# Optimization experiments

Measured on AMD Instinct MI355X. Metric: run time of the kernel, lower is better.

The kernel has to match this reference:

```python
import jax, jax.numpy as jnp
import numpy as np
from jax import lax

RATIO = 0.25
RADIUS = 0.2
NSAMPLE = 32


def _fps(xyz, S):
    # xyz: [B, N, 3] -> indices [B, S] via farthest point sampling (start at 0)
    B, N, _ = xyz.shape

    def body(carry, _):
        dist, farthest = carry  # dist [B,N], farthest [B]
        centroid = jnp.take_along_axis(xyz, farthest[:, None, None], axis=1)  # [B,1,3]
        d = jnp.sum((xyz - centroid) ** 2, axis=-1)  # [B,N]
        dist = jnp.minimum(dist, d)
        nxt = jnp.argmax(dist, axis=-1).astype(jnp.int32)
        return (dist, nxt), farthest

    init = (jnp.full((B, N), 1e10, dtype=xyz.dtype), jnp.zeros((B,), jnp.int32))
    _, idx = lax.scan(body, init, None, length=S)  # [S, B]
    return idx.T  # [B, S]


def _ball_query(radius, nsample, xyz, new_xyz):
    # xyz: [B,N,3], new_xyz: [B,S,3] -> neighbor indices [B,S,nsample]
    B, N, _ = xyz.shape
    sqr = jnp.sum((new_xyz[:, :, None, :] - xyz[:, None, :, :]) ** 2, axis=-1)  # [B,S,N]
    arange = jnp.arange(N, dtype=jnp.int32)[None, None, :]
    idx = jnp.where(sqr <= radius * radius, arange, N)  # out-of-ball -> sentinel N
    idx = jnp.sort(idx, axis=-1)[:, :, :nsample]  # first nsample in-ball points
    first = idx[:, :, :1]
    idx = jnp.where(idx == N, first, idx)  # pad with first valid neighbor
    return idx


def reference(xyz, features, w1, b1, w2, b2, w3, b3):
    # xyz: [B,N,3]; features unused in the non-group_all branch (faithful to source).
    B, N, _ = xyz.shape
    S = int(RATIO * N)

    fps_idx = _fps(xyz, S)  # [B,S]
    new_xyz = jnp.take_along_axis(xyz, fps_idx[:, :, None], axis=1)  # [B,S,3]

    nbr_idx = _ball_query(RADIUS, NSAMPLE, xyz, new_xyz)  # [B,S,K]
    b_idx = jnp.arange(B, dtype=jnp.int32)[:, None, None]
    grouped = xyz[b_idx, nbr_idx]  # [B,S,K,3]
    rel = grouped - new_xyz[:, :, None, :]  # center-relative coords

    # new_points.permute(0,3,2,1): [B,S,K,C] -> [B,C,K,S]; shared 1x1 conv MLP + ReLU
    x = rel.transpose(0, 3, 2, 1)  # [B,3,K,S]
    x = jax.nn.relu(jnp.einsum('bcks,oc->boks', x, w1) + b1[None, :, None, None])
    x = jax.nn.relu(jnp.einsum('bcks,oc->boks', x, w2) + b2[None, :, None, None])
    x = jax.nn.relu(jnp.einsum('bcks,oc->boks', x, w3) + b3[None, :, None, None])

    new_points = jnp.max(x, axis=2)  # max over nsample -> [B,128,S]
    return new_xyz.transpose(0, 2, 1), new_points  # [B,3,S], [B,128,S]


def setup_inputs() -> dict:
    key = jax.random.key(0)
    ks = jax.random.split(key, 8)
    B, N = 8, 8192
    xyz = jax.random.uniform(ks[0], (B, N, 3), dtype=jnp.float32)
    features = jax.random.normal(ks[1], (B, 64, N), dtype=jnp.float32)
    w1 = jax.random.normal(ks[2], (64, 3), dtype=jnp.float32) * (1.0 / np.sqrt(3))
    b1 = jnp.zeros((64,), jnp.float32)
    w2 = jax.random.normal(ks[3], (64, 64), dtype=jnp.float32) * (1.0 / np.sqrt(64))
    b2 = jnp.zeros((64,), jnp.float32)
    w3 = jax.random.normal(ks[4], (128, 64), dtype=jnp.float32) * (1.0 / np.sqrt(64))
    b3 = jnp.zeros((128,), jnp.float32)
    return {"xyz": xyz, "features": features, "w1": w1, "b1": b1,
            "w2": w2, "b2": b2, "w3": w3, "b3": b3}
```

## Files before the change

### kernel.cpp

```cpp
#include <hip/hip_runtime.h>
#include <cstdint>
#include <cstddef>

#define BB 8
#define NN 8192
#define SS 2048
#define KNB 32

typedef float f32x2 __attribute__((ext_vector_type(2)));

__device__ __forceinline__ float sqdist_exact(float ax, float ay, float az,
                                              float bx, float by, float bz) {
#pragma clang fp contract(off)
    float dx = ax - bx;
    float dy = ay - by;
    float dz = az - bz;
    return (dx * dx + dy * dy) + dz * dz;
}

__device__ __forceinline__ f32x2 sqdist2_exact(f32x2 px, f32x2 py, f32x2 pz,
                                               f32x2 cx2, f32x2 cy2, f32x2 cz2) {
#pragma clang fp contract(off)
    f32x2 dx = px - cx2;
    f32x2 dy = py - cy2;
    f32x2 dz = pz - cz2;
    return (dx * dx + dy * dy) + dz * dz;
}

__device__ __forceinline__ unsigned long long u64max(unsigned long long a,
                                                     unsigned long long b) {
    return (a > b) ? a : b;
}

template <int CTRL>
__device__ __forceinline__ unsigned long long dpp_u64max_step(unsigned long long k) {
    int lo = __builtin_amdgcn_update_dpp(0, (int)(unsigned)(k & 0xffffffffu),
                                         CTRL, 0xf, 0xf, false);
    int hi = __builtin_amdgcn_update_dpp(0, (int)(unsigned)(k >> 32),
                                         CTRL, 0xf, 0xf, false);
    unsigned long long o = ((unsigned long long)(unsigned)hi << 32) | (unsigned)lo;
    return (o > k) ? o : k;
}
#define ROW_SHR1 0x111
#define ROW_SHR2 0x112
#define ROW_SHR4 0x114
#define ROW_SHR8 0x118
#define ROW_BC15 0x142
#define ROW_BC31 0x143

__device__ __forceinline__ void wave_minmax(float x, float& lo, float& hi) {
    float a = x, b = x;
#pragma unroll
    for (int off = 1; off < 64; off <<= 1) {
        a = fminf(a, __shfl_xor(a, off));
        b = fmaxf(b, __shfl_xor(b, off));
    }
    lo = a;
    hi = b;
}

__global__ void prep_kernel(const float* __restrict__ w1, const float* __restrict__ w2,
                            const float* __restrict__ w3, float* __restrict__ w1T,
                            float* __restrict__ w2T, float* __restrict__ w3T) {
    for (int i = threadIdx.x; i < 192; i += 256) {
        int oc = i / 3, c = i % 3;
        w1T[c * 64 + oc] = w1[i];
    }
    for (int i = threadIdx.x; i < 4096; i += 256) {
        int oc = i >> 6, j = i & 63;
        w2T[j * 64 + oc] = w2[i];
    }
    for (int i = threadIdx.x; i < 8192; i += 256) {
        int oc = i >> 6, j = i & 63;
        w3T[j * 128 + oc] = w3[i];
    }
}

__device__ __forceinline__ int part3(int v) {
    return (v & 1) | ((v & 2) << 2) | ((v & 4) << 4);
}

#define P4_LIST(X) X(0) X(1) X(2) X(3)

__global__ __attribute__((amdgpu_flat_work_group_size(1024, 1024),
                          amdgpu_waves_per_eu(4, 4)))
void fps_kernel(const float* __restrict__ xyz_all,
                float4* __restrict__ wsSorted,
                float4* __restrict__ wsCtr,
                float* __restrict__ out0) {
    const int b = blockIdx.x;
    const float* xyz = xyz_all + (size_t)b * NN * 3;
    float4* sorted = wsSorted + (size_t)b * NN;
    float4* ctr = wsCtr + (size_t)b * SS;
    float* o0 = out0 + (size_t)b * 3 * SS;

    __shared__ float xLds[NN];
    __shared__ float yLds[NN];
    __shared__ float zLds[NN];
    __shared__ float4 ctrLds[SS];
    __shared__ int cellCnt[512];
    __shared__ int cellBase[512];
    __shared__ unsigned long long red[2][16];

    const int tid = threadIdx.x;
    const int wid = tid >> 6;
    const int lane = tid & 63;

    if (tid < 512) cellCnt[tid] = 0;
    __syncthreads();
    int cellReg[8];
#pragma unroll
    for (int j = 0; j < 8; ++j) {
        int p = tid + j * 1024;
        float x = xyz[p * 3 + 0], y = xyz[p * 3 + 1], z = xyz[p * 3 + 2];
        xLds[p] = x; yLds[p] = y; zLds[p] = z;
        int qx = min(7, (int)(x * 8.0f));
        int qy = min(7, (int)(y * 8.0f));
        int qz = min(7, (int)(z * 8.0f));
        cellReg[j] = part3(qx) | (part3(qy) << 1) | (part3(qz) << 2);
        atomicAdd(&cellCnt[cellReg[j]], 1);
    }
    __syncthreads();
    int myCnt = (tid < 512) ? cellCnt[tid] : 0;
    for (int off = 1; off < 512; off <<= 1) {
        int v = (tid < 512 && tid >= off) ? cellCnt[tid - off] : 0;
        __syncthreads();
        if (tid < 512) cellCnt[tid] += v;
        __syncthreads();
    }
    if (tid < 512) cellBase[tid] = cellCnt[tid] - myCnt;
    __syncthreads();
#pragma unroll
    for (int j = 0; j < 8; ++j) {
        int p = tid + j * 1024;
        float x = xLds[p], y = yLds[p], z = zLds[p];
        int pos = atomicAdd(&cellBase[cellReg[j]], 1);
        sorted[pos] = make_float4(x, y, z, __int_as_float(p));
    }
    __threadfence();
    __syncthreads();

#define DECL_PR(j)                                                   \
    f32x2 px##j, py##j, pz##j, dist##j;                              \
    int ndA##j, ndB##j;                                              \
    {                                                                \
        float4 va = sorted[(wid * 8 + 2 * j) * 64 + lane];           \
        float4 vb = sorted[(wid * 8 + 2 * j + 1) * 64 + lane];       \
        px##j = (f32x2){va.x, vb.x};                                 \
        py##j = (f32x2){va.y, vb.y};                                 \
        pz##j = (f32x2){va.z, vb.z};                                 \
        ndA##j = ~__float_as_int(va.w);                              \
        ndB##j = ~__float_as_int(vb.w);                              \
        dist##j = (f32x2){1e10f, 1e10f};                             \
    }
    P4_LIST(DECL_PR)

    float bbxlo = 0.f, bbxhi = 0.f, bbylo = 0.f, bbyhi = 0.f,
          bbzlo = 0.f, bbzhi = 0.f;
#define BRICK_BB2(j)                                              \
    {                                                             \
        float xl, xh, yl, yh, zl, zh;                             \
        wave_minmax(px##j.x, xl, xh);                             \
        wave_minmax(py##j.x, yl, yh);                             \
        wave_minmax(pz##j.x, zl, zh);                             \
        if (lane == 2 * j) {                                      \
            bbxlo = xl; bbxhi = xh;                               \
            bbylo = yl; bbyhi = yh;                               \
            bbzlo = zl; bbzhi = zh;                               \
        }                                                         \
        wave_minmax(px##j.y, xl, xh);                             \
        wave_minmax(py##j.y, yl, yh);                             \
        wave_minmax(pz##j.y, zl, zh);                             \
        if (lane == 2 * j + 1) {                                  \
            bbxlo = xl; bbxhi = xh;                               \
            bbylo = yl; bbyhi = yh;                               \
            bbzlo = zl; bbzhi = zh;                               \
        }                                                         \
    }
    P4_LIST(BRICK_BB2)

    float cx = xLds[0], cy = yLds[0], cz = zLds[0];
    if (tid == 0) ctrLds[0] = make_float4(cx, cy, cz, 0.0f);

    unsigned long long waveKey =
        ((unsigned long long)__float_as_uint(1e10f) << 32) | 0xFFFFFFFFull;
    float wave_bv = 1e10f;

    for (int s = 1; s < SS; ++s) {
        const int par = s & 1;
        float ddx = fmaxf(fmaxf(bbxlo - cx, cx - bbxhi), 0.0f);
        float ddy = fmaxf(fmaxf(bbylo - cy, cy - bbyhi), 0.0f);
        float ddz = fmaxf(fmaxf(bbzlo - cz, cz - bbzhi), 0.0f);
        float lb2 = (ddx * ddx + ddy * ddy) + ddz * ddz;
        bool act = (lane < 8) && (lb2 * 0.999f < wave_bv);
        if (__ballot(act)) {
            const f32x2 c2x = (f32x2){cx, cx};
            const f32x2 c2y = (f32x2){cy, cy};
            const f32x2 c2z = (f32x2){cz, cz};
#define UPD_PR(j)                                                        \
    {                                                                    \
        f32x2 d = sqdist2_exact(px##j, py##j, pz##j, c2x, c2y, c2z);     \
        dist##j.x = fminf(dist##j.x, d.x);                               \
        dist##j.y = fminf(dist##j.y, d.y);                               \
    }
            P4_LIST(UPD_PR)
#define KEY_PR(j)                                                        \
    unsigned long long kA##j =                                           \
        ((unsigned long long)__float_as_uint(dist##j.x) << 32) |         \
        (unsigned)ndA##j;                                                \
    unsigned long long kB##j =                                           \
        ((unsigned long long)__float_as_uint(dist##j.y) << 32) |         \
        (unsigned)ndB##j;
            P4_LIST(KEY_PR)
            unsigned long long t0 = u64max(kA0, kB0), t1 = u64max(kA1, kB1),
                               t2 = u64max(kA2, kB2), t3 = u64max(kA3, kB3);
            unsigned long long K = u64max(u64max(t0, t1), u64max(t2, t3));
            K = dpp_u64max_step<ROW_SHR1>(K);
            K = dpp_u64max_step<ROW_SHR2>(K);
            K = dpp_u64max_step<ROW_SHR4>(K);
            K = dpp_u64max_step<ROW_SHR8>(K);
            K = dpp_u64max_step<ROW_BC15>(K);
            K = dpp_u64max_step<ROW_BC31>(K);
            if (lane == 63) red[par][wid] = K;
            unsigned wlo = (unsigned)__builtin_amdgcn_readlane(
                (int)(unsigned)(K & 0xffffffffu), 63);
            unsigned whi = (unsigned)__builtin_amdgcn_readlane(
                (int)(unsigned)(K >> 32), 63);
            waveKey = ((unsigned long long)whi << 32) | wlo;
            wave_bv = __int_as_float((int)whi);
        } else {
            if (lane == 0) red[par][wid] = waveKey;
        }
        __syncthreads();
        unsigned long long k = red[par][lane & 15];
        k = dpp_u64max_step<ROW_SHR1>(k);
        k = dpp_u64max_step<ROW_SHR2>(k);
        k = dpp_u64max_step<ROW_SHR4>(k);
        k = dpp_u64max_step<ROW_SHR8>(k);
        unsigned blo = (unsigned)__builtin_amdgcn_readlane(
            (int)(unsigned)(k & 0xffffffffu), 15);
        int wiu = (int)(~blo);
        cx = xLds[wiu];
        cy = yLds[wiu];
        cz = zLds[wiu];
        if (tid == 0) ctrLds[s] = make_float4(cx, cy, cz, 0.0f);
    }

    __syncthreads();
    for (int s = tid; s < SS; s += 1024) {
        float4 c = ctrLds[s];
        o0[s] = c.x;
        o0[SS + s] = c.y;
        o0[2 * SS + s] = c.z;
        ctr[s] = c;
    }
}

__global__ __launch_bounds__(128) void bqmlp_kernel(const float* __restrict__ xyz_all,
                                                    const float4* __restrict__ wsCtr,
                                                    const float* __restrict__ w1T,
                                                    const float* __restrict__ b1,
                                                    const float* __restrict__ w2T,
                                                    const float* __restrict__ b2,
                                                    const float* __restrict__ w3T,
                                                    const float* __restrict__ b3,
                                                    float* __restrict__ out1) {
    const int b = blockIdx.x >> 10;
    const int s0 = (blockIdx.x & 1023) * 2;
    const float* xyz = xyz_all + (size_t)b * NN * 3;

    __shared__ float relF[2 * KNB * 3];
    __shared__ float hT[64 * 64];

    const int tid = threadIdx.x;
    const int cb = __builtin_amdgcn_readfirstlane(tid >> 6);
    const int l = tid & 63;

    {
        float4 cc = wsCtr[(size_t)b * SS + s0 + cb];
        float ccx = cc.x, ccy = cc.y, ccz = cc.z;
        const float R2 = (float)(0.2 * 0.2);
        int total = 0;
        float fx = 0.f, fy = 0.f, fz = 0.f;
        bool have = false;
        for (int chunk = 0; chunk < 128 && total < KNB; ++chunk) {
            int p = chunk * 64 + l;
            float x = xyz[p * 3 + 0], y = xyz[p * 3 + 1], z = xyz[p * 3 + 2];
            float d = sqdist_exact(ccx, ccy, ccz, x, y, z);
            bool hit = (d <= R2);
            unsigned long long mask = __ballot(hit);
            int cnt = __popcll(mask);
            if (cnt) {
                int pos = total + __popcll(mask & ((1ull << l) - 1ull));
                float rx = x - ccx, ry = y - ccy, rz = z - ccz;
                if (hit && pos < KNB) {
                    relF[(cb * KNB + pos) * 3 + 0] = rx;
                    relF[(cb * KNB + pos) * 3 + 1] = ry;
                    relF[(cb * KNB + pos) * 3 + 2] = rz;
                }
                if (hit && pos == 0) { fx = rx; fy = ry; fz = rz; have = true; }
                total += cnt;
            }
        }
        unsigned long long hm = __ballot(have);
        if (total < KNB) {
            int src = __ffsll((long long)hm) - 1;
            float gx = __shfl(fx, src), gy = __shfl(fy, src), gz = __shfl(fz, src);
            if (l >= total && l < KNB) {
                relF[(cb * KNB + l) * 3 + 0] = gx;
                relF[(cb * KNB + l) * 3 + 1] = gy;
                relF[(cb * KNB + l) * 3 + 2] = gz;
            }
        }
    }
    __syncthreads();

    const int r = l;

    {
        float rx = relF[r * 3 + 0], ry = relF[r * 3 + 1], rz = relF[r * 3 + 2];
#pragma unroll
        for (int i = 0; i < 32; ++i) {
            int ch = cb * 32 + i;
            float h = b1[ch];
            h = fmaf(rx, w1T[0 * 64 + ch], h);
            h = fmaf(ry, w1T[1 * 64 + ch], h);
            h = fmaf(rz, w1T[2 * 64 + ch], h);
            hT[ch * 64 + r] = fmaxf(h, 0.0f);
        }
    }
    __syncthreads();

    {
        float acc[32];
#pragma unroll
        for (int i = 0; i < 32; ++i) acc[i] = b2[cb * 32 + i];
#pragma unroll 4
        for (int j = 0; j < 64; ++j) {
            float a = hT[j * 64 + r];
            const float4* wrow = (const float4*)(w2T + j * 64 + cb * 32);
#pragma unroll
            for (int i4 = 0; i4 < 8; ++i4) {
                float4 w = wrow[i4];
                acc[i4 * 4 + 0] = fmaf(a, w.x, acc[i4 * 4 + 0]);
                acc[i4 * 4 + 1] = fmaf(a, w.y, acc[i4 * 4 + 1]);
                acc[i4 * 4 + 2] = fmaf(a, w.z, acc[i4 * 4 + 2]);
                acc[i4 * 4 + 3] = fmaf(a, w.w, acc[i4 * 4 + 3]);
            }
        }
        __syncthreads();
#pragma unroll
        for (int i = 0; i < 32; ++i) hT[(cb * 32 + i) * 64 + r] = fmaxf(acc[i], 0.0f);
    }
    __syncthreads();

    {
        float acc[64];
#pragma unroll
        for (int i = 0; i < 64; ++i) acc[i] = b3[cb * 64 + i];
#pragma unroll 2
        for (int j = 0; j < 64; ++j) {
            float a = hT[j * 64 + r];
            const float4* wrow = (const float4*)(w3T + j * 128 + cb * 64);
#pragma unroll
            for (int i4 = 0; i4 < 16; ++i4) {
                float4 w = wrow[i4];
                acc[i4 * 4 + 0] = fmaf(a, w.x, acc[i4 * 4 + 0]);
                acc[i4 * 4 + 1] = fmaf(a, w.y, acc[i4 * 4 + 1]);
                acc[i4 * 4 + 2] = fmaf(a, w.z, acc[i4 * 4 + 2]);
                acc[i4 * 4 + 3] = fmaf(a, w.w, acc[i4 * 4 + 3]);
            }
        }
#pragma unroll
        for (int i = 0; i < 64; ++i) {
            float v = fmaxf(acc[i], 0.0f);
            v = fmaxf(v, __shfl_xor(v, 1));
            v = fmaxf(v, __shfl_xor(v, 2));
            v = fmaxf(v, __shfl_xor(v, 4));
            v = fmaxf(v, __shfl_xor(v, 8));
            v = fmaxf(v, __shfl_xor(v, 16));
            acc[i] = v;
        }
        if ((l & 31) == 0) {
            int sA = s0 + (l >> 5);
            float* op = out1 + ((size_t)b * 128 + cb * 64) * SS + sA;
#pragma unroll
            for (int i = 0; i < 64; ++i) op[(size_t)i * SS] = acc[i];
        }
    }
}

extern "C" void kernel_launch(void* const* d_in, const int* in_sizes, int n_in,
                              void* d_out, int out_size, void* d_ws, size_t ws_size,
                              hipStream_t stream) {
    (void)in_sizes; (void)n_in; (void)out_size; (void)ws_size;
    const float* xyz = (const float*)d_in[0];
    const float* w1 = (const float*)d_in[2];
    const float* b1 = (const float*)d_in[3];
    const float* w2 = (const float*)d_in[4];
    const float* b2 = (const float*)d_in[5];
    const float* w3 = (const float*)d_in[6];
    const float* b3 = (const float*)d_in[7];
    float* out = (float*)d_out;

    float4* wsCtr = (float4*)d_ws;
    float4* wsSorted = wsCtr + BB * SS;
    float* w1T = (float*)(wsSorted + BB * NN);
    float* w2T = w1T + 192;
    float* w3T = w2T + 4096;

    prep_kernel<<<1, 256, 0, stream>>>(w1, w2, w3, w1T, w2T, w3T);
    fps_kernel<<<BB, 1024, 0, stream>>>(xyz, wsSorted, wsCtr, out);
    bqmlp_kernel<<<BB * (SS / 2), 128, 0, stream>>>(xyz, wsCtr, w1T, b1, w2T, b2,
                                                    w3T, b3, out + BB * 3 * SS);
}
```

Baseline: 1.882 ms.

## Fuse FPS and ball-query MLP into persistent kernel with progress-flag streaming

Merges the FPS kernel and the ball-query/MLP kernel into one persistent launch of 256 blocks. Eight blocks run FPS and publish per-batch progress counters every 16 centroids, while the other blocks pull tasks from an atomic queue and spin-wait until their centroids are ready. This overlaps the MLP stage with the serial FPS stage instead of running them back to back. The change adds spin-wait and atomic overhead, drops the waves_per_eu hint on the FPS path, and relies on all blocks being co-resident to avoid deadlock.

After: 1.752 ms. 6.9% less time.

```diff
diff --git a/kernel.cpp b/kernel.cpp
--- a/kernel.cpp
+++ b/kernel.cpp
@@ -6,6 +6,7 @@
 #define NN 8192
 #define SS 2048
 #define KNB 32
+#define NTASKS (BB * (SS / 16))
 
 typedef float f32x2 __attribute__((ext_vector_type(2)));
 
@@ -61,7 +62,9 @@
 
 __global__ void prep_kernel(const float* __restrict__ w1, const float* __restrict__ w2,
                             const float* __restrict__ w3, float* __restrict__ w1T,
-                            float* __restrict__ w2T, float* __restrict__ w3T) {
+                            float* __restrict__ w2T, float* __restrict__ w3T,
+                            int* __restrict__ syncWs) {
+    if (threadIdx.x < 12) syncWs[threadIdx.x] = 0;
     for (int i = threadIdx.x; i < 192; i += 256) {
         int oc = i / 3, c = i % 3;
         w1T[c * 64 + oc] = w1[i];
@@ -82,311 +85,349 @@
 
 #define P4_LIST(X) X(0) X(1) X(2) X(3)
 
-__global__ __attribute__((amdgpu_flat_work_group_size(1024, 1024),
-                          amdgpu_waves_per_eu(4, 4)))
-void fps_kernel(const float* __restrict__ xyz_all,
-                float4* __restrict__ wsSorted,
-                float4* __restrict__ wsCtr,
-                float* __restrict__ out0) {
-    const int b = blockIdx.x;
-    const float* xyz = xyz_all + (size_t)b * NN * 3;
-    float4* sorted = wsSorted + (size_t)b * NN;
-    float4* ctr = wsCtr + (size_t)b * SS;
-    float* o0 = out0 + (size_t)b * 3 * SS;
-
-    __shared__ float xLds[NN];
-    __shared__ float yLds[NN];
-    __shared__ float zLds[NN];
-    __shared__ float4 ctrLds[SS];
-    __shared__ int cellCnt[512];
-    __shared__ int cellBase[512];
-    __shared__ unsigned long long red[2][16];
+__device__ __forceinline__ void consume_tasks(
+    char* smemRaw, int* taskS, const float* __restrict__ xyz_all,
+    const float4* __restrict__ wsCtr, const float* __restrict__ w1T,
+    const float* __restrict__ b1, const float* __restrict__ w2T,
+    const float* __restrict__ b2, const float* __restrict__ w3T,
+    const float* __restrict__ b3, float* __restrict__ out1,
+    int* __restrict__ prog, int* __restrict__ taskCtr) {
+    const int tid = threadIdx.x;
+    const int l = tid & 63;
+    const int sub = tid >> 7;
+    const int cb = __builtin_amdgcn_readfirstlane((tid >> 6) & 1);
+    float* hT = ((float*)smemRaw) + sub * 4096;
+    float* relF = ((float*)smemRaw) + 8 * 4096 + sub * 192;
+
+    for (;;) {
+        if (tid == 0) *taskS = atomicAdd(taskCtr, 1);
+        __syncthreads();
+        const int t = *taskS;
+        if (t >= NTASKS) break;
+        const int bb = t >> 7;
+        const int base = (t & 127) << 4;
+        if (tid == 0) {
+            while (atomicAdd(&prog[bb], 0) < base + 16) __builtin_amdgcn_s_sleep(16);
+        }
+        __syncthreads();
+        __threadfence();
+        const int s0 = base + sub * 2;
+        const float* xyz = xyz_all + (size_t)bb * NN * 3;
+
+        {
+            float4 cc = wsCtr[(size_t)bb * SS + s0 + cb];
+            float ccx = cc.x, ccy = cc.y, ccz = cc.z;
+            const float R2 = (float)(0.2 * 0.2);
+            int total = 0;
+            float fx = 0.f, fy = 0.f, fz = 0.f;
+            bool have = false;
+            for (int chunk = 0; chunk < 128 && total < KNB; ++chunk) {
+                int p = chunk * 64 + l;
+                float x = xyz[p * 3 + 0], y = xyz[p * 3 + 1], z = xyz[p * 3 + 2];
+                float d = sqdist_exact(ccx, ccy, ccz, x, y, z);
+                bool hit = (d <= R2);
+                unsigned long long mask = __ballot(hit);
+                int cnt = __popcll(mask);
+                if (cnt) {
+                    int pos = total + __popcll(mask & ((1ull << l) - 1ull));
+                    float rx = x - ccx, ry = y - ccy, rz = z - ccz;
+                    if (hit && pos < KNB) {
+                        relF[(cb * KNB + pos) * 3 + 0] = rx;
+                        relF[(cb * KNB + pos) * 3 + 1] = ry;
+                        relF[(cb * KNB + pos) * 3 + 2] = rz;
+                    }
+                    if (hit && pos == 0) { fx = rx; fy = ry; fz = rz; have = true; }
+                    total += cnt;
+                }
+            }
+            unsigned long long hm = __ballot(have);
+            if (total < KNB) {
+                int src = __ffsll((long long)hm) - 1;
+                float gx = __shfl(fx, src), gy = __shfl(fy, src), gz = __shfl(fz, src);
+                if (l >= total && l < KNB) {
+                    relF[(cb * KNB + l) * 3 + 0] = gx;
+                    relF[(cb * KNB + l) * 3 + 1] = gy;
+                    relF[(cb * KNB + l) * 3 + 2] = gz;
+                }
+            }
+        }
+        __syncthreads();
+
+        const int r = l;
+
+        {
+            float rx = relF[r * 3 + 0], ry = relF[r * 3 + 1], rz = relF[r * 3 + 2];
+#pragma unroll
+            for (int i = 0; i < 32; ++i) {
+                int ch = cb * 32 + i;
+                float h = b1[ch];
+                h = fmaf(rx, w1T[0 * 64 + ch], h);
+                h = fmaf(ry, w1T[1 * 64 + ch], h);
+                h = fmaf(rz, w1T[2 * 64 + ch], h);
+                hT[ch * 64 + r] = fmaxf(h, 0.0f);
+            }
+        }
+        __syncthreads();
+
+        {
+            float acc[32];
+#pragma unroll
+            for (int i = 0; i < 32; ++i) acc[i] = b2[cb * 32 + i];
+#pragma unroll 2
+            for (int j = 0; j < 64; ++j) {
+                float a = hT[j * 64 + r];
+                const float4* wrow = (const float4*)(w2T + j * 64 + cb * 32);
+#pragma unroll
+                for (int i4 = 0; i4 < 8; ++i4) {
+                    float4 w = wrow[i4];
+                    acc[i4 * 4 + 0] = fmaf(a, w.x, acc[i4 * 4 + 0]);
+                    acc[i4 * 4 + 1] = fmaf(a, w.y, acc[i4 * 4 + 1]);
+                    acc[i4 * 4 + 2] = fmaf(a, w.z, acc[i4 * 4 + 2]);
+                    acc[i4 * 4 + 3] = fmaf(a, w.w, acc[i4 * 4 + 3]);
+                }
+            }
+            __syncthreads();
+#pragma unroll
+            for (int i = 0; i < 32; ++i) hT[(cb * 32 + i) * 64 + r] = fmaxf(acc[i], 0.0f);
+        }
+        __syncthreads();
+
+#pragma unroll 1
+        for (int half = 0; half < 2; ++half) {
+            float acc[32];
+#pragma unroll
+            for (int i = 0; i < 32; ++i) acc[i] = b3[cb * 64 + half * 32 + i];
+#pragma unroll 2
+            for (int j = 0; j < 64; ++j) {
+                float a = hT[j * 64 + r];
+                const float4* wrow = (const float4*)(w3T + j * 128 + cb * 64 + half * 32);
+#pragma unroll
+                for (int i4 = 0; i4 < 8; ++i4) {
+                    float4 w = wrow[i4];
+                    acc[i4 * 4 + 0] = fmaf(a, w.x, acc[i4 * 4 + 0]);
+                    acc[i4 * 4 + 1] = fmaf(a, w.y, acc[i4 * 4 + 1]);
+                    acc[i4 * 4 + 2] = fmaf(a, w.z, acc[i4 * 4 + 2]);
+                    acc[i4 * 4 + 3] = fmaf(a, w.w, acc[i4 * 4 + 3]);
+                }
+            }
+#pragma unroll
+            for (int i = 0; i < 32; ++i) {
+                float v = fmaxf(acc[i], 0.0f);
+                v = fmaxf(v, __shfl_xor(v, 1));
+                v = fmaxf(v, __shfl_xor(v, 2));
+                v = fmaxf(v, __shfl_xor(v, 4));
+                v = fmaxf(v, __shfl_xor(v, 8));
+                v = fmaxf(v, __shfl_xor(v, 16));
+                acc[i] = v;
+            }
+            if ((l & 31) == 0) {
+                int sA = s0 + (l >> 5);
+                float* op = out1 + ((size_t)bb * 128 + cb * 64 + half * 32) * SS + sA;
+#pragma unroll
+                for (int i = 0; i < 32; ++i) op[(size_t)i * SS] = acc[i];
+            }
+        }
+        __syncthreads();
+    }
+}
+
+__global__ __attribute__((amdgpu_flat_work_group_size(1024, 1024)))
+void fused_kernel(const float* __restrict__ xyz_all,
+                  float4* __restrict__ wsSorted,
+                  float4* __restrict__ wsCtr,
+                  float* __restrict__ out0,
+                  const float* __restrict__ w1T, const float* __restrict__ b1,
+                  const float* __restrict__ w2T, const float* __restrict__ b2,
+                  const float* __restrict__ w3T, const float* __restrict__ b3,
+                  float* __restrict__ out1, int* __restrict__ syncWs) {
+    __shared__ __align__(16) char smemRaw[137216];
+    __shared__ int taskS;
+    int* prog = syncWs;
+    int* taskCtr = syncWs + 8;
 
     const int tid = threadIdx.x;
     const int wid = tid >> 6;
     const int lane = tid & 63;
 
-    if (tid < 512) cellCnt[tid] = 0;
-    __syncthreads();
-    int cellReg[8];
-#pragma unroll
-    for (int j = 0; j < 8; ++j) {
-        int p = tid + j * 1024;
-        float x = xyz[p * 3 + 0], y = xyz[p * 3 + 1], z = xyz[p * 3 + 2];
-        xLds[p] = x; yLds[p] = y; zLds[p] = z;
-        int qx = min(7, (int)(x * 8.0f));
-        int qy = min(7, (int)(y * 8.0f));
-        int qz = min(7, (int)(z * 8.0f));
-        cellReg[j] = part3(qx) | (part3(qy) << 1) | (part3(qz) << 2);
-        atomicAdd(&cellCnt[cellReg[j]], 1);
-    }
-    __syncthreads();
-    int myCnt = (tid < 512) ? cellCnt[tid] : 0;
-    for (int off = 1; off < 512; off <<= 1) {
-        int v = (tid < 512 && tid >= off) ? cellCnt[tid - off] : 0;
-        __syncthreads();
-        if (tid < 512) cellCnt[tid] += v;
-        __syncthreads();
-    }
-    if (tid < 512) cellBase[tid] = cellCnt[tid] - myCnt;
-    __syncthreads();
-#pragma unroll
-    for (int j = 0; j < 8; ++j) {
-        int p = tid + j * 1024;
-        float x = xLds[p], y = yLds[p], z = zLds[p];
-        int pos = atomicAdd(&cellBase[cellReg[j]], 1);
-        sorted[pos] = make_float4(x, y, z, __int_as_float(p));
-    }
-    __threadfence();
-    __syncthreads();
+    if (blockIdx.x < BB) {
+        const int b = blockIdx.x;
+        const float* xyz = xyz_all + (size_t)b * NN * 3;
+        float4* sorted = wsSorted + (size_t)b * NN;
+        float4* ctr = wsCtr + (size_t)b * SS;
+        float* o0 = out0 + (size_t)b * 3 * SS;
+
+        float* xLds = (float*)smemRaw;
+        float* yLds = xLds + NN;
+        float* zLds = yLds + NN;
+        float4* ctrLds = (float4*)(zLds + NN);
+        int* cellCnt = (int*)(ctrLds + SS);
+        int* cellBase = cellCnt + 512;
+        unsigned long long* redp = (unsigned long long*)(cellBase + 512);
+
+        if (tid < 512) cellCnt[tid] = 0;
+        __syncthreads();
+        int cellReg[8];
+#pragma unroll
+        for (int j = 0; j < 8; ++j) {
+            int p = tid + j * 1024;
+            float x = xyz[p * 3 + 0], y = xyz[p * 3 + 1], z = xyz[p * 3 + 2];
+            xLds[p] = x; yLds[p] = y; zLds[p] = z;
+            int qx = min(7, (int)(x * 8.0f));
+            int qy = min(7, (int)(y * 8.0f));
+            int qz = min(7, (int)(z * 8.0f));
+            cellReg[j] = part3(qx) | (part3(qy) << 1) | (part3(qz) << 2);
+            atomicAdd(&cellCnt[cellReg[j]], 1);
+        }
+        __syncthreads();
+        int myCnt = (tid < 512) ? cellCnt[tid] : 0;
+        for (int off = 1; off < 512; off <<= 1) {
+            int v = (tid < 512 && tid >= off) ? cellCnt[tid - off] : 0;
+            __syncthreads();
+            if (tid < 512) cellCnt[tid] += v;
+            __syncthreads();
+        }
+        if (tid < 512) cellBase[tid] = cellCnt[tid] - myCnt;
+        __syncthreads();
+#pragma unroll
+        for (int j = 0; j < 8; ++j) {
+            int p = tid + j * 1024;
+            float x = xLds[p], y = yLds[p], z = zLds[p];
+            int pos = atomicAdd(&cellBase[cellReg[j]], 1);
+            sorted[pos] = make_float4(x, y, z, __int_as_float(p));
+        }
+        __threadfence();
+        __syncthreads();
 
 #define DECL_PR(j)                                                   \
-    f32x2 px##j, py##j, pz##j, dist##j;                              \
-    int ndA##j, ndB##j;                                              \
-    {                                                                \
-        float4 va = sorted[(wid * 8 + 2 * j) * 64 + lane];           \
-        float4 vb = sorted[(wid * 8 + 2 * j + 1) * 64 + lane];       \
-        px##j = (f32x2){va.x, vb.x};                                 \
-        py##j = (f32x2){va.y, vb.y};                                 \
-        pz##j = (f32x2){va.z, vb.z};                                 \
-        ndA##j = ~__float_as_int(va.w);                              \
-        ndB##j = ~__float_as_int(vb.w);                              \
-        dist##j = (f32x2){1e10f, 1e10f};                             \
-    }
-    P4_LIST(DECL_PR)
-
-    float bbxlo = 0.f, bbxhi = 0.f, bbylo = 0.f, bbyhi = 0.f,
-          bbzlo = 0.f, bbzhi = 0.f;
+        f32x2 px##j, py##j, pz##j, dist##j;                          \
+        int ndA##j, ndB##j;                                          \
+        {                                                            \
+            float4 va = sorted[(wid * 8 + 2 * j) * 64 + lane];       \
+            float4 vb = sorted[(wid * 8 + 2 * j + 1) * 64 + lane];   \
+            px##j = (f32x2){va.x, vb.x};                             \
+            py##j = (f32x2){va.y, vb.y};                             \
+            pz##j = (f32x2){va.z, vb.z};                             \
+            ndA##j = ~__float_as_int(va.w);                          \
+            ndB##j = ~__float_as_int(vb.w);                          \
+            dist##j = (f32x2){1e10f, 1e10f};                         \
+        }
+        P4_LIST(DECL_PR)
+
+        float bbxlo = 0.f, bbxhi = 0.f, bbylo = 0.f, bbyhi = 0.f,
+              bbzlo = 0.f, bbzhi = 0.f;
 #define BRICK_BB2(j)                                              \
-    {                                                             \
-        float xl, xh, yl, yh, zl, zh;                             \
-        wave_minmax(px##j.x, xl, xh);                             \
-        wave_minmax(py##j.x, yl, yh);                             \
-        wave_minmax(pz##j.x, zl, zh);                             \
-        if (lane == 2 * j) {                                      \
-            bbxlo = xl; bbxhi = xh;                               \
-            bbylo = yl; bbyhi = yh;                               \
-            bbzlo = zl; bbzhi = zh;                               \
-        }                                                         \
-        wave_minmax(px##j.y, xl, xh);                             \
-        wave_minmax(py##j.y, yl, yh);                             \
-        wave_minmax(pz##j.y, zl, zh);                             \
-        if (lane == 2 * j + 1) {                                  \
-            bbxlo = xl; bbxhi = xh;                               \
-            bbylo = yl; bbyhi = yh;                               \
-            bbzlo = zl; bbzhi = zh;                               \
-        }                                                         \
-    }
-    P4_LIST(BRICK_BB2)
-
-    float cx = xLds[0], cy = yLds[0], cz = zLds[0];
-    if (tid == 0) ctrLds[0] = make_float4(cx, cy, cz, 0.0f);
-
-    unsigned long long waveKey =
-        ((unsigned long long)__float_as_uint(1e10f) << 32) | 0xFFFFFFFFull;
-    float wave_bv = 1e10f;
-
-    for (int s = 1; s < SS; ++s) {
-        const int par = s & 1;
-        float ddx = fmaxf(fmaxf(bbxlo - cx, cx - bbxhi), 0.0f);
-        float ddy = fmaxf(fmaxf(bbylo - cy, cy - bbyhi), 0.0f);
-        float ddz = fmaxf(fmaxf(bbzlo - cz, cz - bbzhi), 0.0f);
-        float lb2 = (ddx * ddx + ddy * ddy) + ddz * ddz;
-        bool act = (lane < 8) && (lb2 * 0.999f < wave_bv);
-        if (__ballot(act)) {
-            const f32x2 c2x = (f32x2){cx, cx};
-            const f32x2 c2y = (f32x2){cy, cy};
-            const f32x2 c2z = (f32x2){cz, cz};
+        {                                                         \
+            float xl, xh, yl, yh, zl, zh;                         \
+            wave_minmax(px##j.x, xl, xh);                         \
+            wave_minmax(py##j.x, yl, yh);                         \
+            wave_minmax(pz##j.x, zl, zh);                         \
+            if (lane == 2 * j) {                                  \
+                bbxlo = xl; bbxhi = xh;                           \
+                bbylo = yl; bbyhi = yh;                           \
+                bbzlo = zl; bbzhi = zh;                           \
+            }                                                     \
+            wave_minmax(px##j.y, xl, xh);                         \
+            wave_minmax(py##j.y, yl, yh);                         \
+            wave_minmax(pz##j.y, zl, zh);                         \
+            if (lane == 2 * j + 1) {                              \
+                bbxlo = xl; bbxhi = xh;                           \
+                bbylo = yl; bbyhi = yh;                           \
+                bbzlo = zl; bbzhi = zh;                           \
+            }                                                     \
+        }
+        P4_LIST(BRICK_BB2)
+
+        float cx = xLds[0], cy = yLds[0], cz = zLds[0];
+        if (tid == 0) {
+            float4 c4 = make_float4(cx, cy, cz, 0.0f);
+            ctrLds[0] = c4;
+            ctr[0] = c4;
+        }
+
+        unsigned long long waveKey =
+            ((unsigned long long)__float_as_uint(1e10f) << 32) | 0xFFFFFFFFull;
+        float wave_bv = 1e10f;
+
+        for (int s = 1; s < SS; ++s) {
+            const int par = s & 1;
+            float ddx = fmaxf(fmaxf(bbxlo - cx, cx - bbxhi), 0.0f);
+            float ddy = fmaxf(fmaxf(bbylo - cy, cy - bbyhi), 0.0f);
+            float ddz = fmaxf(fmaxf(bbzlo - cz, cz - bbzhi), 0.0f);
+            float lb2 = (ddx * ddx + ddy * ddy) + ddz * ddz;
+            bool act = (lane < 8) && (lb2 * 0.999f < wave_bv);
+            if (__ballot(act)) {
+                const f32x2 c2x = (f32x2){cx, cx};
+                const f32x2 c2y = (f32x2){cy, cy};
+                const f32x2 c2z = (f32x2){cz, cz};
 #define UPD_PR(j)                                                        \
-    {                                                                    \
-        f32x2 d = sqdist2_exact(px##j, py##j, pz##j, c2x, c2y, c2z);     \
-        dist##j.x = fminf(dist##j.x, d.x);                               \
-        dist##j.y = fminf(dist##j.y, d.y);                               \
-    }
-            P4_LIST(UPD_PR)
+                {                                                        \
+                    f32x2 d = sqdist2_exact(px##j, py##j, pz##j, c2x, c2y, c2z); \
+                    dist##j.x = fminf(dist##j.x, d.x);                   \
+                    dist##j.y = fminf(dist##j.y, d.y);                   \
+                }
+                P4_LIST(UPD_PR)
 #define KEY_PR(j)                                                        \
-    unsigned long long kA##j =                                           \
-        ((unsigned long long)__float_as_uint(dist##j.x) << 32) |         \
-        (unsigned)ndA##j;                                                \
-    unsigned long long kB##j =                                           \
-        ((unsigned long long)__float_as_uint(dist##j.y) << 32) |         \
-        (unsigned)ndB##j;
-            P4_LIST(KEY_PR)
-            unsigned long long t0 = u64max(kA0, kB0), t1 = u64max(kA1, kB1),
-                               t2 = u64max(kA2, kB2), t3 = u64max(kA3, kB3);
-            unsigned long long K = u64max(u64max(t0, t1), u64max(t2, t3));
-            K = dpp_u64max_step<ROW_SHR1>(K);
-            K = dpp_u64max_step<ROW_SHR2>(K);
-            K = dpp_u64max_step<ROW_SHR4>(K);
-            K = dpp_u64max_step<ROW_SHR8>(K);
-            K = dpp_u64max_step<ROW_BC15>(K);
-            K = dpp_u64max_step<ROW_BC31>(K);
-            if (lane == 63) red[par][wid] = K;
-            unsigned wlo = (unsigned)__builtin_amdgcn_readlane(
-                (int)(unsigned)(K & 0xffffffffu), 63);
-            unsigned whi = (unsigned)__builtin_amdgcn_readlane(
-                (int)(unsigned)(K >> 32), 63);
-            waveKey = ((unsigned long long)whi << 32) | wlo;
-            wave_bv = __int_as_float((int)whi);
-        } else {
-            if (lane == 0) red[par][wid] = waveKey;
-        }
-        __syncthreads();
-        unsigned long long k = red[par][lane & 15];
-        k = dpp_u64max_step<ROW_SHR1>(k);
-        k = dpp_u64max_step<ROW_SHR2>(k);
-        k = dpp_u64max_step<ROW_SHR4>(k);
-        k = dpp_u64max_step<ROW_SHR8>(k);
-        unsigned blo = (unsigned)__builtin_amdgcn_readlane(
-            (int)(unsigned)(k & 0xffffffffu), 15);
-        int wiu = (int)(~blo);
-        cx = xLds[wiu];
-        cy = yLds[wiu];
-        cz = zLds[wiu];
-        if (tid == 0) ctrLds[s] = make_float4(cx, cy, cz, 0.0f);
-    }
-
-    __syncthreads();
-    for (int s = tid; s < SS; s += 1024) {
-        float4 c = ctrLds[s];
-        o0[s] = c.x;
-        o0[SS + s] = c.y;
-        o0[2 * SS + s] = c.z;
-        ctr[s] = c;
-    }
-}
-
-__global__ __launch_bounds__(128) void bqmlp_kernel(const float* __restrict__ xyz_all,
-                                                    const float4* __restrict__ wsCtr,
-                                                    const float* __restrict__ w1T,
-                                                    const float* __restrict__ b1,
-                                                    const float* __restrict__ w2T,
-                                                    const float* __restrict__ b2,
-                                                    const float* __restrict__ w3T,
-                                                    const float* __restrict__ b3,
-                                                    float* __restrict__ out1) {
-    const int b = blockIdx.x >> 10;
-    const int s0 = (blockIdx.x & 1023) * 2;
-    const float* xyz = xyz_all + (size_t)b * NN * 3;
-
-    __shared__ float relF[2 * KNB * 3];
-    __shared__ float hT[64 * 64];
-
-    const int tid = threadIdx.x;
-    const int cb = __builtin_amdgcn_readfirstlane(tid >> 6);
-    const int l = tid & 63;
-
-    {
-        float4 cc = wsCtr[(size_t)b * SS + s0 + cb];
-        float ccx = cc.x, ccy = cc.y, ccz = cc.z;
-        const float R2 = (float)(0.2 * 0.2);
-        int total = 0;
-        float fx = 0.f, fy = 0.f, fz = 0.f;
-        bool have = false;
-        for (int chunk = 0; chunk < 128 && total < KNB; ++chunk) {
-            int p = chunk * 64 + l;
-            float x = xyz[p * 3 + 0], y = xyz[p * 3 + 1], z = xyz[p * 3 + 2];
-            float d = sqdist_exact(ccx, ccy, ccz, x, y, z);
-            bool hit = (d <= R2);
-            unsigned long long mask = __ballot(hit);
-            int cnt = __popcll(mask);
-            if (cnt) {
-                int pos = total + __popcll(mask & ((1ull << l) - 1ull));
-                float rx = x - ccx, ry = y - ccy, rz = z - ccz;
-                if (hit && pos < KNB) {
-                    relF[(cb * KNB + pos) * 3 + 0] = rx;
-                    relF[(cb * KNB + pos) * 3 + 1] = ry;
-                    relF[(cb * KNB + pos) * 3 + 2] = rz;
-                }
-                if (hit && pos == 0) { fx = rx; fy = ry; fz = rz; have = true; }
-                total += cnt;
-            }
-        }
-        unsigned long long hm = __ballot(have);
-        if (total < KNB) {
-            int src = __ffsll((long long)hm) - 1;
-            float gx = __shfl(fx, src), gy = __shfl(fy, src), gz = __shfl(fz, src);
-            if (l >= total && l < KNB) {
-                relF[(cb * KNB + l) * 3 + 0] = gx;
-                relF[(cb * KNB + l) * 3 + 1] = gy;
-                relF[(cb * KNB + l) * 3 + 2] = gz;
-            }
-        }
-    }
-    __syncthreads();
-
-    const int r = l;
-
-    {
-        float rx = relF[r * 3 + 0], ry = relF[r * 3 + 1], rz = relF[r * 3 + 2];
-#pragma unroll
-        for (int i = 0; i < 32; ++i) {
-            int ch = cb * 32 + i;
-            float h = b1[ch];
-            h = fmaf(rx, w1T[0 * 64 + ch], h);
-            h = fmaf(ry, w1T[1 * 64 + ch], h);
-            h = fmaf(rz, w1T[2 * 64 + ch], h);
-            hT[ch * 64 + r] = fmaxf(h, 0.0f);
-        }
-    }
-    __syncthreads();
-
-    {
-        float acc[32];
-#pragma unroll
-        for (int i = 0; i < 32; ++i) acc[i] = b2[cb * 32 + i];
-#pragma unroll 4
-        for (int j = 0; j < 64; ++j) {
-            float a = hT[j * 64 + r];
-            const float4* wrow = (const float4*)(w2T + j * 64 + cb * 32);
-#pragma unroll
-            for (int i4 = 0; i4 < 8; ++i4) {
-                float4 w = wrow[i4];
-                acc[i4 * 4 + 0] = fmaf(a, w.x, acc[i4 * 4 + 0]);
-                acc[i4 * 4 + 1] = fmaf(a, w.y, acc[i4 * 4 + 1]);
-                acc[i4 * 4 + 2] = fmaf(a, w.z, acc[i4 * 4 + 2]);
-                acc[i4 * 4 + 3] = fmaf(a, w.w, acc[i4 * 4 + 3]);
-            }
-        }
-        __syncthreads();
-#pragma unroll
-        for (int i = 0; i < 32; ++i) hT[(cb * 32 + i) * 64 + r] = fmaxf(acc[i], 0.0f);
-    }
-    __syncthreads();
-
-    {
-        float acc[64];
-#pragma unroll
-        for (int i = 0; i < 64; ++i) acc[i] = b3[cb * 64 + i];
-#pragma unroll 2
-        for (int j = 0; j < 64; ++j) {
-            float a = hT[j * 64 + r];
-            const float4* wrow = (const float4*)(w3T + j * 128 + cb * 64);
-#pragma unroll
-            for (int i4 = 0; i4 < 16; ++i4) {
-                float4 w = wrow[i4];
-                acc[i4 * 4 + 0] = fmaf(a, w.x, acc[i4 * 4 + 0]);
-                acc[i4 * 4 + 1] = fmaf(a, w.y, acc[i4 * 4 + 1]);
-                acc[i4 * 4 + 2] = fmaf(a, w.z, acc[i4 * 4 + 2]);
-                acc[i4 * 4 + 3] = fmaf(a, w.w, acc[i4 * 4 + 3]);
-            }
-        }
-#pragma unroll
-        for (int i = 0; i < 64; ++i) {
-            float v = fmaxf(acc[i], 0.0f);
-            v = fmaxf(v, __shfl_xor(v, 1));
-            v = fmaxf(v, __shfl_xor(v, 2));
-            v = fmaxf(v, __shfl_xor(v, 4));
-            v = fmaxf(v, __shfl_xor(v, 8));
-            v = fmaxf(v, __shfl_xor(v, 16));
-            acc[i] = v;
-        }
-        if ((l & 31) == 0) {
-            int sA = s0 + (l >> 5);
-            float* op = out1 + ((size_t)b * 128 + cb * 64) * SS + sA;
-#pragma unroll
-            for (int i = 0; i < 64; ++i) op[(size_t)i * SS] = acc[i];
-        }
+                unsigned long long kA##j =                               \
+                    ((unsigned long long)__float_as_uint(dist##j.x) << 32) | \
+                    (unsigned)ndA##j;                                    \
+                unsigned long long kB##j =                               \
+                    ((unsigned long long)__float_as_uint(dist##j.y) << 32) | \
+                    (unsigned)ndB##j;
+                P4_LIST(KEY_PR)
+                unsigned long long t0 = u64max(kA0, kB0), t1 = u64max(kA1, kB1),
+                                   t2 = u64max(kA2, kB2), t3 = u64max(kA3, kB3);
+                unsigned long long K = u64max(u64max(t0, t1), u64max(t2, t3));
+                K = dpp_u64max_step<ROW_SHR1>(K);
+                K = dpp_u64max_step<ROW_SHR2>(K);
+                K = dpp_u64max_step<ROW_SHR4>(K);
+                K = dpp_u64max_step<ROW_SHR8>(K);
+                K = dpp_u64max_step<ROW_BC15>(K);
+                K = dpp_u64max_step<ROW_BC31>(K);
+                if (lane == 63) redp[par * 16 + wid] = K;
+                unsigned wlo = (unsigned)__builtin_amdgcn_readlane(
+                    (int)(unsigned)(K & 0xffffffffu), 63);
+                unsigned whi = (unsigned)__builtin_amdgcn_readlane(
+                    (int)(unsigned)(K >> 32), 63);
+                waveKey = ((unsigned long long)whi << 32) | wlo;
+                wave_bv = __int_as_float((int)whi);
+            } else {
+                if (lane == 0) redp[par * 16 + wid] = waveKey;
+            }
+            __syncthreads();
+            unsigned long long k = redp[par * 16 + (lane & 15)];
+            k = dpp_u64max_step<ROW_SHR1>(k);
+            k = dpp_u64max_step<ROW_SHR2>(k);
+            k = dpp_u64max_step<ROW_SHR4>(k);
+            k = dpp_u64max_step<ROW_SHR8>(k);
+            unsigned blo = (unsigned)__builtin_amdgcn_readlane(
+                (int)(unsigned)(k & 0xffffffffu), 15);
+            int wiu = (int)(~blo);
+            cx = xLds[wiu];
+            cy = yLds[wiu];
+            cz = zLds[wiu];
+            if (tid == 0) {
+                float4 c4 = make_float4(cx, cy, cz, 0.0f);
+                ctrLds[s] = c4;
+                ctr[s] = c4;
+            }
+            if ((s & 15) == 15 && wid == 0) {
+                __threadfence();
+                if (lane == 0) atomicExch(&prog[b], s + 1);
+            }
+        }
+
+        __syncthreads();
+        for (int s = tid; s < SS; s += 1024) {
+            float4 c = ctrLds[s];
+            o0[s] = c.x;
+            o0[SS + s] = c.y;
+            o0[2 * SS + s] = c.z;
+        }
+        consume_tasks(smemRaw, &taskS, xyz_all, wsCtr, w1T, b1, w2T, b2,
+                      w3T, b3, out1, prog, taskCtr);
+    } else {
+        consume_tasks(smemRaw, &taskS, xyz_all, wsCtr, w1T, b1, w2T, b2,
+                      w3T, b3, out1, prog, taskCtr);
     }
 }
 
@@ -408,9 +449,10 @@
     float* w1T = (float*)(wsSorted + BB * NN);
     float* w2T = w1T + 192;
     float* w3T = w2T + 4096;
-
-    prep_kernel<<<1, 256, 0, stream>>>(w1, w2, w3, w1T, w2T, w3T);
-    fps_kernel<<<BB, 1024, 0, stream>>>(xyz, wsSorted, wsCtr, out);
-    bqmlp_kernel<<<BB * (SS / 2), 128, 0, stream>>>(xyz, wsCtr, w1T, b1, w2T, b2,
-                                                    w3T, b3, out + BB * 3 * SS);
-}
+    int* syncWs = (int*)(w3T + 8192);
+
+    prep_kernel<<<1, 256, 0, stream>>>(w1, w2, w3, w1T, w2T, w3T, syncWs);
+    fused_kernel<<<256, 1024, 0, stream>>>(xyz, wsSorted, wsCtr, out,
+                                           w1T, b1, w2T, b2, w3T, b3,
+                                           out + BB * 3 * SS, syncWs);
+}
```
